# Kernel optimization log

Hardware: AMD Instinct MI355X
Metric: run time of the kernel (lower is better)

Reference implementation:

```python
import jax, jax.numpy as jnp
import numpy as np
from jax import lax

KERNEL_SIZE = 10
WEIGHT = 1.0


def setup_inputs() -> dict:
    key = jax.random.key(0)
    # NHWC segmentation score map: [batch, H, W, n_classes]
    inputs = jax.random.uniform(key, (16, 512, 512, 8), dtype=jnp.float32)
    return {"inputs": inputs}


def reference(inputs) -> jnp.ndarray:
    # tf.nn.erosion2d with a flat (all-zero) structuring element == sliding-window min
    # tf.nn.dilation2d with a flat kernel == sliding-window max
    # SAME padding: erosion pads with +inf (identity of min), dilation with -inf.
    k = KERNEL_SIZE
    window = (1, k, k, 1)
    strides = (1, 1, 1, 1)
    eroded = lax.reduce_window(inputs, jnp.float32(jnp.inf), lax.min,
                               window, strides, "SAME")
    opened = lax.reduce_window(eroded, jnp.float32(-jnp.inf), lax.max,
                               window, strides, "SAME")
    return opened * jnp.float32(WEIGHT)
```

## Files before the change

### kernel.cpp

```cpp
#include <hip/hip_runtime.h>
#include <math.h>


#define W_F4   1024
#define IMG_F4 (512 * W_F4)
#define TH     31
#define TW     32
#define RA     40
#define CA     100
#define S_A    101
#define CB     82
#define NJ     41

__device__ __forceinline__ float4 f4min(float4 a, float4 b) {
    return make_float4(fminf(a.x,b.x), fminf(a.y,b.y), fminf(a.z,b.z), fminf(a.w,b.w));
}
__device__ __forceinline__ float4 f4max(float4 a, float4 b) {
    return make_float4(fmaxf(a.x,b.x), fmaxf(a.y,b.y), fmaxf(a.z,b.z), fmaxf(a.w,b.w));
}

__global__ __launch_bounds__(512, 4) void opening(const float4* __restrict__ in,
                                                  float4* __restrict__ out) {
    __shared__ float4 sA[RA * S_A];

    const float4 pinf4 = make_float4( INFINITY,  INFINITY,  INFINITY,  INFINITY);
    const float4 ninf4 = make_float4(-INFINITY, -INFINITY, -INFINITY, -INFINITY);

    const int t  = threadIdx.x;
    const int h0 = blockIdx.y * TH;
    const int w0 = blockIdx.x * TW;

    const float4* img  = in  + (size_t)blockIdx.z * IMG_F4;
    float4*       oimg = out + (size_t)blockIdx.z * IMG_F4;

    if (t < 5 * CA) {
        const int c = t % CA;
        const int p = t / CA;
        const int colf4 = w0 * 2 - 16 + c;
        const bool colok = (colf4 >= 0) & (colf4 < W_F4);

        float4 v[17];
#pragma unroll
        for (int q = 0; q < 17; q++) {
            int h = h0 + p * 8 + q - 8;
            bool ok = colok & (h >= 0) & (h < 512);
            v[q] = ok ? img[(size_t)h * W_F4 + colf4] : pinf4;
        }
        float4 L[9]; L[8] = v[8];
#pragma unroll
        for (int i = 7; i >= 0; i--) L[i] = f4min(v[i], L[i + 1]);
        float4 rr = v[9];
#pragma unroll
        for (int i = 0; i < 8; i++) {
            if (i > 0) rr = f4min(rr, v[9 + i]);
            sA[(p * 8 + i) * S_A + c] = f4min(L[i], rr);
        }
    }
    __syncthreads();

    {
        const bool act = t < 2 * RA * 6;
        int base = 0, j0 = 0;
        float4 o8[8];
        if (act) {
            const int c4 = t & 1;
            const int r  = (t >> 1) % RA;
            j0 = ((t >> 1) / RA) * 8;
            base = r * S_A + c4;
            float4 L[9]; L[8] = sA[base + 2 * (j0 + 8)];
#pragma unroll
            for (int i = 7; i >= 0; i--) L[i] = f4min(sA[base + 2 * (j0 + i)], L[i + 1]);
            float4 rr;
#pragma unroll
            for (int i = 0; i < 8; i++) {
                int k = j0 + 9 + i;
                float4 tap = (k < 50) ? sA[base + 2 * k] : pinf4;
                rr = i ? f4min(rr, tap) : tap;
                o8[i] = f4min(L[i], rr);
            }
        }
        __syncthreads();
        if (act) {
#pragma unroll
            for (int i = 0; i < 8; i++) {
                int j = j0 + i;
                if (j < NJ) sA[base + 2 * j] = o8[i];
            }
        }
    }
    __syncthreads();

    {
        const bool act = t < CB * 4;
        int c = 0, o0 = 0;
        float4 o8[8];
        if (act) {
            c  = t % CB;
            o0 = (t / CB) * 8;
            float4 L[9];
#pragma unroll
            for (int i = 8; i >= 0; i--) {
                int s = o0 + i;
                int h = h0 - 4 + s;
                float4 tap = ((h >= 0) & (h < 512)) ? sA[s * S_A + c] : ninf4;
                L[i] = (i == 8) ? tap : f4max(tap, L[i + 1]);
            }
            float4 rr;
#pragma unroll
            for (int i = 0; i < 8; i++) {
                int s = o0 + 9 + i;
                int h = h0 - 4 + s;
                float4 tap = ((s < RA) & (h >= 0) & (h < 512)) ? sA[s * S_A + c] : ninf4;
                rr = i ? f4max(rr, tap) : tap;
                o8[i] = f4max(L[i], rr);
            }
        }
        __syncthreads();
        if (act) {
#pragma unroll
            for (int i = 0; i < 8; i++) {
                int o = o0 + i;
                if (o < TH) sA[o * S_A + c] = o8[i];
            }
        }
    }
    __syncthreads();

    {
        const bool act = t < 2 * TH * 4;
        int base = 0, x0 = 0;
        float4 o8[8];
        if (act) {
            const int c4 = t & 1;
            const int r  = (t >> 1) % TH;
            x0 = ((t >> 1) / TH) * 8;
            base = r * S_A + c4;
            float4 L[9];
#pragma unroll
            for (int i = 8; i >= 0; i--) {
                int j = x0 + i;
                int px = w0 - 4 + j;
                float4 tap = ((px >= 0) & (px < 512)) ? sA[base + 2 * j] : ninf4;
                L[i] = (i == 8) ? tap : f4max(tap, L[i + 1]);
            }
            float4 rr;
#pragma unroll
            for (int i = 0; i < 8; i++) {
                int j = x0 + 9 + i;
                int px = w0 - 4 + j;
                float4 tap = ((px >= 0) & (px < 512)) ? sA[base + 2 * j] : ninf4;
                rr = i ? f4max(rr, tap) : tap;
                o8[i] = f4max(L[i], rr);
            }
        }
        __syncthreads();
        if (act) {
#pragma unroll
            for (int i = 0; i < 8; i++)
                sA[base + 2 * (x0 + i)] = o8[i];
        }
    }
    __syncthreads();

    for (int idx = t; idx < TH * 64; idx += 512) {
        int r = idx >> 6;
        int c = idx & 63;
        int h = h0 + r;
        if (h < 512)
            oimg[(size_t)h * W_F4 + (size_t)(w0 * 2 + c)] = sA[r * S_A + c];
    }
}

extern "C" void kernel_launch(void* const* d_in, const int* in_sizes, int n_in,
                              void* d_out, int out_size, void* d_ws, size_t ws_size,
                              hipStream_t stream) {
    const float4* in  = (const float4*)d_in[0];
    float4*       out = (float4*)d_out;
    (void)d_ws; (void)ws_size;

    dim3 grid(512 / TW, (512 + TH - 1) / TH, 16);
    opening<<<grid, 512, 0, stream>>>(in, out);
}
```

Measured before the change: 315.5 us.

## Process 16 outputs per thread in van Herk passes and specialise interior tiles

Adds a templated van Herk/Gil-Werman helper that produces up to 16 outputs per thread by reusing a second prefix/suffix block, instead of 8 outputs per thread. Each of the four separable passes now uses fewer threads with more work each, which cuts redundant tap loads from global memory and LDS. Interior tiles skip per-tap boundary checks through yin/xin fast paths. The cost is higher register pressure under launch bounds of 512x4 and fewer active threads per phase, which reduces latency hiding.

```diff
diff --git a/kernel.cpp b/kernel.cpp
--- a/kernel.cpp
+++ b/kernel.cpp
@@ -9,7 +9,6 @@
 #define RA     40
 #define CA     100
 #define S_A    101
-#define CB     82
 #define NJ     41
 
 __device__ __forceinline__ float4 f4min(float4 a, float4 b) {
@@ -17,6 +16,46 @@
 }
 __device__ __forceinline__ float4 f4max(float4 a, float4 b) {
     return make_float4(fmaxf(a.x,b.x), fmaxf(a.y,b.y), fmaxf(a.z,b.z), fmaxf(a.w,b.w));
+}
+template<bool MIN>
+__device__ __forceinline__ float4 f4op(float4 a, float4 b) {
+    return MIN ? f4min(a, b) : f4max(a, b);
+}
+
+template<int R, bool MIN, class F>
+__device__ __forceinline__ void gw_run(F tap, float4* o) {
+    float4 v8, L[9];
+    {
+        float4 v[9];
+#pragma unroll
+        for (int q = 0; q < 9; q++) v[q] = tap(q);
+        v8 = v[8];
+        L[8] = v[8];
+#pragma unroll
+        for (int i = 7; i >= 0; i--) L[i] = f4op<MIN>(v[i], L[i + 1]);
+    }
+    float4 w[8], rr;
+#pragma unroll
+    for (int i = 0; i < 8; i++) {
+        float4 tv = tap(9 + i);
+        w[i] = tv;
+        rr = i ? f4op<MIN>(rr, tv) : tv;
+        o[i] = f4op<MIN>(L[i], rr);
+    }
+    if (R > 8) {
+        float4 L2[9];
+        L2[8] = w[7];
+#pragma unroll
+        for (int i = 7; i >= 1; i--) L2[i] = f4op<MIN>(w[i - 1], L2[i + 1]);
+        L2[0] = f4op<MIN>(v8, L2[1]);
+        float4 r2;
+#pragma unroll
+        for (int i = 0; i < R - 8; i++) {
+            float4 tv = tap(17 + i);
+            r2 = i ? f4op<MIN>(r2, tv) : tv;
+            o[8 + i] = f4op<MIN>(L2[i], r2);
+        }
+    }
 }
 
 __global__ __launch_bounds__(512, 4) void opening(const float4* __restrict__ in,
@@ -29,135 +68,137 @@
     const int t  = threadIdx.x;
     const int h0 = blockIdx.y * TH;
     const int w0 = blockIdx.x * TW;
+    const bool yin = (h0 >= 8) && (h0 + RA < 512);
+    const bool xin = (w0 >= 8) && (2 * w0 + 83 < W_F4);
 
     const float4* img  = in  + (size_t)blockIdx.z * IMG_F4;
     float4*       oimg = out + (size_t)blockIdx.z * IMG_F4;
 
-    if (t < 5 * CA) {
-        const int c = t % CA;
-        const int p = t / CA;
-        const int colf4 = w0 * 2 - 16 + c;
-        const bool colok = (colf4 >= 0) & (colf4 < W_F4);
-
-        float4 v[17];
-#pragma unroll
-        for (int q = 0; q < 17; q++) {
-            int h = h0 + p * 8 + q - 8;
-            bool ok = colok & (h >= 0) & (h < 512);
-            v[q] = ok ? img[(size_t)h * W_F4 + colf4] : pinf4;
-        }
-        float4 L[9]; L[8] = v[8];
-#pragma unroll
-        for (int i = 7; i >= 0; i--) L[i] = f4min(v[i], L[i + 1]);
-        float4 rr = v[9];
-#pragma unroll
-        for (int i = 0; i < 8; i++) {
-            if (i > 0) rr = f4min(rr, v[9 + i]);
-            sA[(p * 8 + i) * S_A + c] = f4min(L[i], rr);
-        }
-    }
-    __syncthreads();
-
-    {
-        const bool act = t < 2 * RA * 6;
+    if (t < 3 * 128) {
+        const int p  = t >> 7;
+        const int id = t & 127;
+        if (id < CA) {
+            const int s0    = p * 16;
+            const int hbase = h0 - 8 + s0;
+            const int colf4 = w0 * 2 - 16 + id;
+            float4 o[16];
+            if (yin) {
+                const bool colok = (colf4 >= 0) & (colf4 < W_F4);
+                if (colok) {
+                    auto tap = [&](int q) { return img[(size_t)(hbase + q) * W_F4 + colf4]; };
+                    if (p < 2) {
+                        gw_run<16, true>(tap, o);
+#pragma unroll
+                        for (int i = 0; i < 16; i++) sA[(s0 + i) * S_A + id] = o[i];
+                    } else {
+                        gw_run<8, true>(tap, o);
+#pragma unroll
+                        for (int i = 0; i < 8; i++) sA[(s0 + i) * S_A + id] = o[i];
+                    }
+                } else {
+                    const int Rn = (p < 2) ? 16 : 8;
+                    for (int i = 0; i < Rn; i++) sA[(s0 + i) * S_A + id] = pinf4;
+                }
+            } else {
+                auto tap = [&](int q) {
+                    int h = hbase + q;
+                    bool ok = (colf4 >= 0) & (colf4 < W_F4) & (h >= 0) & (h < 512);
+                    return ok ? img[(size_t)h * W_F4 + colf4] : pinf4;
+                };
+                if (p < 2) {
+                    gw_run<16, true>(tap, o);
+#pragma unroll
+                    for (int i = 0; i < 16; i++) sA[(s0 + i) * S_A + id] = o[i];
+                } else {
+                    gw_run<8, true>(tap, o);
+#pragma unroll
+                    for (int i = 0; i < 8; i++) sA[(s0 + i) * S_A + id] = o[i];
+                }
+            }
+        }
+    }
+    __syncthreads();
+
+    {
+        const int u  = t >> 7;
+        const int id = t & 127;
+        const bool act = (t < 3 * 128) && (id < 2 * RA);
         int base = 0, j0 = 0;
-        float4 o8[8];
-        if (act) {
-            const int c4 = t & 1;
-            const int r  = (t >> 1) % RA;
-            j0 = ((t >> 1) / RA) * 8;
-            base = r * S_A + c4;
-            float4 L[9]; L[8] = sA[base + 2 * (j0 + 8)];
-#pragma unroll
-            for (int i = 7; i >= 0; i--) L[i] = f4min(sA[base + 2 * (j0 + i)], L[i + 1]);
-            float4 rr;
-#pragma unroll
-            for (int i = 0; i < 8; i++) {
-                int k = j0 + 9 + i;
-                float4 tap = (k < 50) ? sA[base + 2 * k] : pinf4;
-                rr = i ? f4min(rr, tap) : tap;
-                o8[i] = f4min(L[i], rr);
+        float4 o[14];
+        if (act) {
+            base = (id >> 1) * S_A + (id & 1);
+            j0 = u * 14;
+            auto tap = [&](int q) { return sA[base + 2 * (j0 + q)]; };
+            if (u < 2) gw_run<14, true>(tap, o);
+            else       gw_run<13, true>(tap, o);
+        }
+        __syncthreads();
+        if (act) {
+#pragma unroll
+            for (int i = 0; i < 14; i++)
+                sA[base + 2 * (j0 + i)] = o[i];
+        }
+    }
+    __syncthreads();
+
+    {
+        const int u  = t >> 7;
+        const int id = t & 127;
+        const bool act = (t < 2 * 128) && (id < 82);
+        int c = 0, o0 = 0;
+        float4 o[16];
+        if (act) {
+            c  = id;
+            o0 = u * 16;
+            if (yin) {
+                auto tap = [&](int q) { return sA[(o0 + q) * S_A + c]; };
+                gw_run<16, false>(tap, o);
+            } else {
+                auto tap = [&](int q) {
+                    int s = o0 + q;
+                    float4 val = sA[s * S_A + c];
+                    int h = h0 - 4 + s;
+                    return ((h >= 0) & (h < 512)) ? val : ninf4;
+                };
+                gw_run<16, false>(tap, o);
             }
         }
         __syncthreads();
         if (act) {
 #pragma unroll
-            for (int i = 0; i < 8; i++) {
-                int j = j0 + i;
-                if (j < NJ) sA[base + 2 * j] = o8[i];
+            for (int i = 0; i < 16; i++)
+                sA[(o0 + i) * S_A + c] = o[i];
+        }
+    }
+    __syncthreads();
+
+    {
+        const int u  = t >> 6;
+        const int id = t & 63;
+        const bool act = (t < 2 * 64) && (id < 2 * TH);
+        int base = 0, x0 = 0;
+        float4 o[16];
+        if (act) {
+            base = (id >> 1) * S_A + (id & 1);
+            x0 = u * 16;
+            if (xin) {
+                auto tap = [&](int q) { return sA[base + 2 * (x0 + q)]; };
+                gw_run<16, false>(tap, o);
+            } else {
+                auto tap = [&](int q) {
+                    int j = x0 + q;
+                    float4 val = sA[base + 2 * j];
+                    int px = w0 - 4 + j;
+                    return ((px >= 0) & (px < 512)) ? val : ninf4;
+                };
+                gw_run<16, false>(tap, o);
             }
         }
-    }
-    __syncthreads();
-
-    {
-        const bool act = t < CB * 4;
-        int c = 0, o0 = 0;
-        float4 o8[8];
-        if (act) {
-            c  = t % CB;
-            o0 = (t / CB) * 8;
-            float4 L[9];
-#pragma unroll
-            for (int i = 8; i >= 0; i--) {
-                int s = o0 + i;
-                int h = h0 - 4 + s;
-                float4 tap = ((h >= 0) & (h < 512)) ? sA[s * S_A + c] : ninf4;
-                L[i] = (i == 8) ? tap : f4max(tap, L[i + 1]);
-            }
-            float4 rr;
-#pragma unroll
-            for (int i = 0; i < 8; i++) {
-                int s = o0 + 9 + i;
-                int h = h0 - 4 + s;
-                float4 tap = ((s < RA) & (h >= 0) & (h < 512)) ? sA[s * S_A + c] : ninf4;
-                rr = i ? f4max(rr, tap) : tap;
-                o8[i] = f4max(L[i], rr);
-            }
-        }
         __syncthreads();
         if (act) {
 #pragma unroll
-            for (int i = 0; i < 8; i++) {
-                int o = o0 + i;
-                if (o < TH) sA[o * S_A + c] = o8[i];
-            }
-        }
-    }
-    __syncthreads();
-
-    {
-        const bool act = t < 2 * TH * 4;
-        int base = 0, x0 = 0;
-        float4 o8[8];
-        if (act) {
-            const int c4 = t & 1;
-            const int r  = (t >> 1) % TH;
-            x0 = ((t >> 1) / TH) * 8;
-            base = r * S_A + c4;
-            float4 L[9];
-#pragma unroll
-            for (int i = 8; i >= 0; i--) {
-                int j = x0 + i;
-                int px = w0 - 4 + j;
-                float4 tap = ((px >= 0) & (px < 512)) ? sA[base + 2 * j] : ninf4;
-                L[i] = (i == 8) ? tap : f4max(tap, L[i + 1]);
-            }
-            float4 rr;
-#pragma unroll
-            for (int i = 0; i < 8; i++) {
-                int j = x0 + 9 + i;
-                int px = w0 - 4 + j;
-                float4 tap = ((px >= 0) & (px < 512)) ? sA[base + 2 * j] : ninf4;
-                rr = i ? f4max(rr, tap) : tap;
-                o8[i] = f4max(L[i], rr);
-            }
-        }
-        __syncthreads();
-        if (act) {
-#pragma unroll
-            for (int i = 0; i < 8; i++)
-                sA[base + 2 * (x0 + i)] = o8[i];
+            for (int i = 0; i < 16; i++)
+                sA[base + 2 * (x0 + i)] = o[i];
         }
     }
     __syncthreads();
@@ -166,7 +207,7 @@
         int r = idx >> 6;
         int c = idx & 63;
         int h = h0 + r;
-        if (h < 512)
+        if (yin || h < 512)
             oimg[(size_t)h * W_F4 + (size_t)(w0 * 2 + c)] = sA[r * S_A + c];
     }
 }
```

After: 255.8 us. 1.23x faster.
